# Kernel optimization log

Hardware: AMD Instinct MI355X
Metric: run time of the kernel (lower is better)

Reference implementation:

```python
import jax, jax.numpy as jnp
import numpy as np

TEMPERATURE = 0.5
NEG_INF = -1e9  # used to mask self-similarity diagonal before logsumexp


def setup_inputs() -> dict:
    key = jax.random.key(0)
    k1, k2 = jax.random.split(key)
    N, Z = 4096, 128
    z1 = jax.random.normal(k1, (N, Z), dtype=jnp.float32)
    z2 = jax.random.normal(k2, (N, Z), dtype=jnp.float32)
    return {"z1": z1, "z2": z2}


def reference(z1, z2):
    # NT-Xent (SimCLR) loss. Faithful to:
    #   sim = cosine_similarity over all pairs of concat([z1, z2])
    #   positives = sim diagonals at offsets +-N; negatives = all off-(self)diag entries
    #   cross_entropy with the positive as class 0  ->  -pos/T + logsumexp(all non-self sims / T)
    N = z1.shape[0]
    reps = jnp.concatenate([z1, z2], axis=0)                      # [2N, Z]
    # row-normalize once; cosine sim matrix is then a single GEMM
    norms = jnp.linalg.norm(reps, axis=-1, keepdims=True)
    # torch cosine_similarity clamps norms by eps=1e-8
    nreps = reps / jnp.maximum(norms, 1e-8)
    sim = nreps @ nreps.T                                          # [2N, 2N]
    # positives: sim[i, i+N] for i<N and sim[i, i-N] for i>=N
    l_pos = jnp.diagonal(sim, offset=N)                            # [N]
    r_pos = jnp.diagonal(sim, offset=-N)                           # [N]
    positives = jnp.concatenate([l_pos, r_pos])                    # [2N]
    # logsumexp over all entries except the self-similarity diagonal.
    # (The positive entry stays in the denominator exactly once, matching
    #  concat([positive, negatives]) in the original.)
    two_n = 2 * N
    self_mask = jnp.eye(two_n, dtype=bool)
    logits = jnp.where(self_mask, NEG_INF, sim / TEMPERATURE)      # [2N, 2N]
    lse = jax.nn.logsumexp(logits, axis=1)                         # [2N]
    per_row = lse - positives / TEMPERATURE                        # CE with label 0
    return jnp.sum(per_row) / two_n
```

## Files before the change

kernel.cpp:

```cpp
#include <hip/hip_runtime.h>
#include <hip/hip_bf16.h>


#define N_PAIRS 4096
#define ZDIM    128
#define NROWS   8192
#define QS 1.6986437717f

typedef __bf16 bf16x8 __attribute__((ext_vector_type(8)));
typedef float  floatx4 __attribute__((ext_vector_type(4)));

__global__ __launch_bounds__(256) void k_normalize(
    const float* __restrict__ z1, const float* __restrict__ z2,
    __hip_bfloat16* __restrict__ pack, float* __restrict__ pos,
    float* __restrict__ denom)
{
    const int zi = blockIdx.x * 256 + threadIdx.x;
    if (zi < NROWS) denom[zi] = 0.0f;

    const int w = threadIdx.x >> 6;
    const int lane = threadIdx.x & 63;
    const int p = blockIdx.x * 4 + w;
    const float2 a = ((const float2*)(z1 + (size_t)p * ZDIM))[lane];
    const float2 b = ((const float2*)(z2 + (size_t)p * ZDIM))[lane];
    float s1 = a.x * a.x + a.y * a.y;
    float s2 = b.x * b.x + b.y * b.y;
    float d  = a.x * b.x + a.y * b.y;
    #pragma unroll
    for (int off = 1; off < 64; off <<= 1) {
        s1 += __shfl_xor(s1, off, 64);
        s2 += __shfl_xor(s2, off, 64);
        d  += __shfl_xor(d,  off, 64);
    }
    const float n1 = fmaxf(sqrtf(s1), 1e-8f);
    const float n2 = fmaxf(sqrtf(s2), 1e-8f);
    const float i1 = 1.0f / n1, i2 = 1.0f / n2;
    const float q1 = i1 * QS, q2 = i2 * QS;
    float2 na; na.x = a.x * q1; na.y = a.y * q1;
    float2 nb; nb.x = b.x * q2; nb.y = b.y * q2;

    const int ks = lane >> 4;
    const int qq = (lane >> 2) & 3;
    const int jj = (lane & 3) * 2;
    const int r1 = p, r2 = p + N_PAIRS;
    const size_t i1e = ((size_t)((r1 >> 4) * 4 + ks)) * 512 + qq * 128 + (r1 & 15) * 8 + jj;
    const size_t i2e = ((size_t)((r2 >> 4) * 4 + ks)) * 512 + qq * 128 + (r2 & 15) * 8 + jj;
    *(__hip_bfloat162*)(pack + i1e) = __float22bfloat162_rn(na);
    *(__hip_bfloat162*)(pack + i2e) = __float22bfloat162_rn(nb);
    if (lane == 0) pos[p] = d * i1 * i2;
}

__global__ __launch_bounds__(256) void k_simsum(
    const __hip_bfloat16* __restrict__ pack, float* __restrict__ denom)
{
    const int tid  = threadIdx.x;
    const int lane = tid & 63;
    const int w    = tid >> 6;
    const int q    = lane >> 4;
    const int l16  = lane & 15;

    const int b  = blockIdx.x;
    int u        = (33 * b) >> 2;
    const int u1 = (33 * b + 33) >> 2;

    int rt = 0, snext = 256;
    while (u >= snext) { ++rt; snext += 256 - 8 * rt; }

    bf16x8 bufA[4][2], bufB[4][2];

    auto loadB = [&](bf16x8 (&buf)[4][2], int col) {
        const __hip_bfloat16* bp = pack + (size_t)col * 128 + lane * 8;
        #pragma unroll
        for (int ks = 0; ks < 4; ++ks)
            #pragma unroll
            for (int nt = 0; nt < 2; ++nt)
                buf[ks][nt] = *(const bf16x8*)(bp + nt * 2048 + ks * 512);
    };

    while (u < u1) {
        const int srt  = snext - (256 - 8 * rt);
        const int uend = (u1 < snext) ? u1 : snext;
        const int rowb = rt * 256 + w * 64;

        const __hip_bfloat16* Abase = pack + (size_t)rowb * 128 + lane * 8;
        bf16x8 afrag[4][4];
        #pragma unroll
        for (int mt = 0; mt < 4; ++mt)
            #pragma unroll
            for (int ks = 0; ks < 4; ++ks)
                afrag[mt][ks] = *(const bf16x8*)(Abase + mt * 2048 + ks * 512);

        float rowsum[4][4];
        #pragma unroll
        for (int mt = 0; mt < 4; ++mt)
            #pragma unroll
            for (int r = 0; r < 4; ++r) rowsum[mt][r] = 0.0f;

        auto compute = [&](bf16x8 (&buf)[4][2], int ur) {
            const int  col  = rt * 256 + ur * 32;
            const bool band = (ur < 8);
            floatx4 acc[4][2];
            #pragma unroll
            for (int mt = 0; mt < 4; ++mt)
                #pragma unroll
                for (int nt = 0; nt < 2; ++nt) {
                    acc[mt][nt].x = 0.f; acc[mt][nt].y = 0.f;
                    acc[mt][nt].z = 0.f; acc[mt][nt].w = 0.f;
                }
            #pragma unroll
            for (int ks = 0; ks < 4; ++ks)
                #pragma unroll
                for (int mt = 0; mt < 4; ++mt)
                    #pragma unroll
                    for (int nt = 0; nt < 2; ++nt)
                        acc[mt][nt] = __builtin_amdgcn_mfma_f32_16x16x32_bf16(
                            afrag[mt][ks], buf[ks][nt], acc[mt][nt], 0, 0, 0);
            float cp0 = 0.0f, cp1 = 0.0f;
            #pragma unroll
            for (int mt = 0; mt < 4; ++mt) {
                const int rowtb = rowb + mt * 16;
                #pragma unroll
                for (int nt = 0; nt < 2; ++nt) {
                    const int coltb = col + nt * 16;
                    if (band && rowtb == coltb) {
                        #pragma unroll
                        for (int r = 0; r < 4; ++r) {
                            const float e = __builtin_amdgcn_exp2f(acc[mt][nt][r]);
                            rowsum[mt][r] += (l16 == q * 4 + r) ? 0.0f : e;
                        }
                    } else {
                        #pragma unroll
                        for (int r = 0; r < 4; ++r) {
                            const float e = __builtin_amdgcn_exp2f(acc[mt][nt][r]);
                            rowsum[mt][r] += e;
                            if (!band) { if (nt == 0) cp0 += e; else cp1 += e; }
                        }
                    }
                }
            }
            if (!band) {
                cp0 += __shfl_xor(cp0, 16, 64);
                cp0 += __shfl_xor(cp0, 32, 64);
                cp1 += __shfl_xor(cp1, 16, 64);
                cp1 += __shfl_xor(cp1, 32, 64);
                if (q == 0) {
                    atomicAdd(&denom[col + l16], cp0);
                    atomicAdd(&denom[col + 16 + l16], cp1);
                }
            }
        };

        int ur        = u - srt;
        const int urn = uend - srt;
        loadB(bufA, rt * 256 + ur * 32);
        while (ur + 2 <= urn) {
            loadB(bufB, rt * 256 + (ur + 1) * 32);
            compute(bufA, ur);
            int nx = ur + 2;
            if (nx >= urn) nx = urn - 1;
            loadB(bufA, rt * 256 + nx * 32);
            compute(bufB, ur + 1);
            ur += 2;
        }
        if (ur < urn) compute(bufA, ur);

        #pragma unroll
        for (int mt = 0; mt < 4; ++mt)
            #pragma unroll
            for (int r = 0; r < 4; ++r) {
                float s = rowsum[mt][r];
                s += __shfl_xor(s, 1, 64);
                s += __shfl_xor(s, 2, 64);
                s += __shfl_xor(s, 4, 64);
                s += __shfl_xor(s, 8, 64);
                rowsum[mt][r] = s;
            }
        if (l16 == 0) {
            #pragma unroll
            for (int mt = 0; mt < 4; ++mt)
                #pragma unroll
                for (int r = 0; r < 4; ++r)
                    atomicAdd(&denom[rowb + mt * 16 + q * 4 + r], rowsum[mt][r]);
        }

        u = uend;
        if (u < u1) { ++rt; snext += 256 - 8 * rt; }
    }
}

__global__ __launch_bounds__(1024) void k_finish(
    const float* __restrict__ denom, const float* __restrict__ pos,
    float* __restrict__ out)
{
    __shared__ float red[16];
    const int t = threadIdx.x;
    const int lane = t & 63, wv = t >> 6;
    float s = 0.0f;
    for (int i = t; i < NROWS; i += 1024) s += __logf(denom[i]);
    float p = 0.0f;
    for (int i = t; i < N_PAIRS; i += 1024) p += pos[i];
    float v = s - 4.0f * p;
    #pragma unroll
    for (int off = 1; off < 64; off <<= 1) v += __shfl_xor(v, off, 64);
    if (lane == 0) red[wv] = v;
    __syncthreads();
    if (wv == 0) {
        float x = (lane < 16) ? red[lane] : 0.0f;
        #pragma unroll
        for (int off = 1; off < 16; off <<= 1) x += __shfl_xor(x, off, 64);
        if (lane == 0) out[0] = x / (float)NROWS;
    }
}

extern "C" void kernel_launch(void* const* d_in, const int* in_sizes, int n_in,
                              void* d_out, int out_size, void* d_ws, size_t ws_size,
                              hipStream_t stream) {
    const float* z1 = (const float*)d_in[0];
    const float* z2 = (const float*)d_in[1];
    float* out = (float*)d_out;

    char* ws = (char*)d_ws;
    __hip_bfloat16* pack = (__hip_bfloat16*)ws;
    float* denom = (float*)(ws + (size_t)NROWS * ZDIM * 2);
    float* pos   = denom + NROWS;

    k_normalize<<<N_PAIRS / 4, 256, 0, stream>>>(z1, z2, pack, pos, denom);
    k_simsum<<<512, 256, 0, stream>>>(pack, denom);
    k_finish<<<1, 1024, 0, stream>>>(denom, pos, out);
}
```

Baseline: 82.14 us.

## Fuse normalize, similarity-sum and finish into one cooperative kernel

Replaces the three kernel launches with a single cooperative kernel of 512 blocks. A grid-wide sync separates normalization from the similarity GEMM, and a last-block-done atomic counter runs the final reduction. The aim is to remove the launch gaps and the inter-kernel drains between stages. In exchange it pays for a grid sync, an extra atomic ticket and fences, and each block now normalizes two pairs per wave. The old three-kernel path remains as a fallback if the cooperative launch fails.

```diff
diff --git a/kernel.cpp b/kernel.cpp
--- a/kernel.cpp
+++ b/kernel.cpp
@@ -1,14 +1,227 @@
 #include <hip/hip_runtime.h>
 #include <hip/hip_bf16.h>
+#include <hip/hip_cooperative_groups.h>
+
+namespace cg = cooperative_groups;
 
 
 #define N_PAIRS 4096
 #define ZDIM    128
 #define NROWS   8192
 #define QS 1.6986437717f
+#define GRID_SIM 512
 
 typedef __bf16 bf16x8 __attribute__((ext_vector_type(8)));
 typedef float  floatx4 __attribute__((ext_vector_type(4)));
+
+__global__ __launch_bounds__(256) void k_fused(
+    const float* __restrict__ z1, const float* __restrict__ z2,
+    __hip_bfloat16* __restrict__ pack, float* __restrict__ pos,
+    float* __restrict__ denom, unsigned int* __restrict__ ctr,
+    float* __restrict__ out)
+{
+    const int tid  = threadIdx.x;
+    const int lane = tid & 63;
+    const int w    = tid >> 6;
+    const int q    = lane >> 4;
+    const int l16  = lane & 15;
+    const int b    = blockIdx.x;
+
+    __shared__ unsigned int tk;
+    __shared__ float red[4];
+
+    {
+        const int zi = b * 256 + tid;
+        if (zi < NROWS) denom[zi] = 0.0f;
+        if (zi == 0) *ctr = 0u;
+
+        #pragma unroll
+        for (int pp = 0; pp < 2; ++pp) {
+            const int p = b * 8 + w * 2 + pp;
+            const float2 a = ((const float2*)(z1 + (size_t)p * ZDIM))[lane];
+            const float2 bb = ((const float2*)(z2 + (size_t)p * ZDIM))[lane];
+            float s1 = a.x * a.x + a.y * a.y;
+            float s2 = bb.x * bb.x + bb.y * bb.y;
+            float d  = a.x * bb.x + a.y * bb.y;
+            #pragma unroll
+            for (int off = 1; off < 64; off <<= 1) {
+                s1 += __shfl_xor(s1, off, 64);
+                s2 += __shfl_xor(s2, off, 64);
+                d  += __shfl_xor(d,  off, 64);
+            }
+            const float n1 = fmaxf(sqrtf(s1), 1e-8f);
+            const float n2 = fmaxf(sqrtf(s2), 1e-8f);
+            const float i1 = 1.0f / n1, i2 = 1.0f / n2;
+            const float q1 = i1 * QS, q2 = i2 * QS;
+            float2 na; na.x = a.x * q1; na.y = a.y * q1;
+            float2 nb; nb.x = bb.x * q2; nb.y = bb.y * q2;
+
+            const int ks = lane >> 4;
+            const int qq = (lane >> 2) & 3;
+            const int jj = (lane & 3) * 2;
+            const int r1 = p, r2 = p + N_PAIRS;
+            const size_t i1e = ((size_t)((r1 >> 4) * 4 + ks)) * 512 + qq * 128 + (r1 & 15) * 8 + jj;
+            const size_t i2e = ((size_t)((r2 >> 4) * 4 + ks)) * 512 + qq * 128 + (r2 & 15) * 8 + jj;
+            *(__hip_bfloat162*)(pack + i1e) = __float22bfloat162_rn(na);
+            *(__hip_bfloat162*)(pack + i2e) = __float22bfloat162_rn(nb);
+            if (lane == 0) pos[p] = d * i1 * i2;
+        }
+    }
+
+    cg::this_grid().sync();
+
+    {
+        int u        = (33 * b) >> 2;
+        const int u1 = (33 * b + 33) >> 2;
+
+        int rt = 0, snext = 256;
+        while (u >= snext) { ++rt; snext += 256 - 8 * rt; }
+
+        bf16x8 bufA[4][2], bufB[4][2];
+
+        auto loadB = [&](bf16x8 (&buf)[4][2], int col) {
+            const __hip_bfloat16* bp = pack + (size_t)col * 128 + lane * 8;
+            #pragma unroll
+            for (int ks = 0; ks < 4; ++ks)
+                #pragma unroll
+                for (int nt = 0; nt < 2; ++nt)
+                    buf[ks][nt] = *(const bf16x8*)(bp + nt * 2048 + ks * 512);
+        };
+
+        while (u < u1) {
+            const int srt  = snext - (256 - 8 * rt);
+            const int uend = (u1 < snext) ? u1 : snext;
+            const int rowb = rt * 256 + w * 64;
+
+            const __hip_bfloat16* Abase = pack + (size_t)rowb * 128 + lane * 8;
+            bf16x8 afrag[4][4];
+            #pragma unroll
+            for (int mt = 0; mt < 4; ++mt)
+                #pragma unroll
+                for (int ks = 0; ks < 4; ++ks)
+                    afrag[mt][ks] = *(const bf16x8*)(Abase + mt * 2048 + ks * 512);
+
+            float rowsum[4][4];
+            #pragma unroll
+            for (int mt = 0; mt < 4; ++mt)
+                #pragma unroll
+                for (int r = 0; r < 4; ++r) rowsum[mt][r] = 0.0f;
+
+            auto compute = [&](bf16x8 (&buf)[4][2], int ur) {
+                const int  col  = rt * 256 + ur * 32;
+                const bool band = (ur < 8);
+                floatx4 acc[4][2];
+                #pragma unroll
+                for (int mt = 0; mt < 4; ++mt)
+                    #pragma unroll
+                    for (int nt = 0; nt < 2; ++nt) {
+                        acc[mt][nt].x = 0.f; acc[mt][nt].y = 0.f;
+                        acc[mt][nt].z = 0.f; acc[mt][nt].w = 0.f;
+                    }
+                #pragma unroll
+                for (int ks = 0; ks < 4; ++ks)
+                    #pragma unroll
+                    for (int mt = 0; mt < 4; ++mt)
+                        #pragma unroll
+                        for (int nt = 0; nt < 2; ++nt)
+                            acc[mt][nt] = __builtin_amdgcn_mfma_f32_16x16x32_bf16(
+                                afrag[mt][ks], buf[ks][nt], acc[mt][nt], 0, 0, 0);
+                float cp0 = 0.0f, cp1 = 0.0f;
+                #pragma unroll
+                for (int mt = 0; mt < 4; ++mt) {
+                    const int rowtb = rowb + mt * 16;
+                    #pragma unroll
+                    for (int nt = 0; nt < 2; ++nt) {
+                        const int coltb = col + nt * 16;
+                        if (band && rowtb == coltb) {
+                            #pragma unroll
+                            for (int r = 0; r < 4; ++r) {
+                                const float e = __builtin_amdgcn_exp2f(acc[mt][nt][r]);
+                                rowsum[mt][r] += (l16 == q * 4 + r) ? 0.0f : e;
+                            }
+                        } else {
+                            #pragma unroll
+                            for (int r = 0; r < 4; ++r) {
+                                const float e = __builtin_amdgcn_exp2f(acc[mt][nt][r]);
+                                rowsum[mt][r] += e;
+                                if (!band) { if (nt == 0) cp0 += e; else cp1 += e; }
+                            }
+                        }
+                    }
+                }
+                if (!band) {
+                    cp0 += __shfl_xor(cp0, 16, 64);
+                    cp0 += __shfl_xor(cp0, 32, 64);
+                    cp1 += __shfl_xor(cp1, 16, 64);
+                    cp1 += __shfl_xor(cp1, 32, 64);
+                    if (q == 0) {
+                        atomicAdd(&denom[col + l16], cp0);
+                        atomicAdd(&denom[col + 16 + l16], cp1);
+                    }
+                }
+            };
+
+            int ur        = u - srt;
+            const int urn = uend - srt;
+            loadB(bufA, rt * 256 + ur * 32);
+            while (ur + 2 <= urn) {
+                loadB(bufB, rt * 256 + (ur + 1) * 32);
+                compute(bufA, ur);
+                int nx = ur + 2;
+                if (nx >= urn) nx = urn - 1;
+                loadB(bufA, rt * 256 + nx * 32);
+                compute(bufB, ur + 1);
+                ur += 2;
+            }
+            if (ur < urn) compute(bufA, ur);
+
+            #pragma unroll
+            for (int mt = 0; mt < 4; ++mt)
+                #pragma unroll
+                for (int r = 0; r < 4; ++r) {
+                    float s = rowsum[mt][r];
+                    s += __shfl_xor(s, 1, 64);
+                    s += __shfl_xor(s, 2, 64);
+                    s += __shfl_xor(s, 4, 64);
+                    s += __shfl_xor(s, 8, 64);
+                    rowsum[mt][r] = s;
+                }
+            if (l16 == 0) {
+                #pragma unroll
+                for (int mt = 0; mt < 4; ++mt)
+                    #pragma unroll
+                    for (int r = 0; r < 4; ++r)
+                        atomicAdd(&denom[rowb + mt * 16 + q * 4 + r], rowsum[mt][r]);
+            }
+
+            u = uend;
+            if (u < u1) { ++rt; snext += 256 - 8 * rt; }
+        }
+    }
+
+    __threadfence();
+    __syncthreads();
+    if (tid == 0) tk = atomicAdd(ctr, 1u);
+    __syncthreads();
+    if (tk == GRID_SIM - 1) {
+        __threadfence();
+        float s = 0.0f;
+        for (int i = tid; i < NROWS; i += 256) s += __logf(denom[i]);
+        float p = 0.0f;
+        for (int i = tid; i < N_PAIRS; i += 256) p += pos[i];
+        float v = s - 4.0f * p;
+        #pragma unroll
+        for (int off = 1; off < 64; off <<= 1) v += __shfl_xor(v, off, 64);
+        if (lane == 0) red[w] = v;
+        __syncthreads();
+        if (w == 0) {
+            float x = (lane < 4) ? red[lane] : 0.0f;
+            x += __shfl_xor(x, 1, 64);
+            x += __shfl_xor(x, 2, 64);
+            if (lane == 0) out[0] = x / (float)NROWS;
+        }
+    }
+}
 
 __global__ __launch_bounds__(256) void k_normalize(
     const float* __restrict__ z1, const float* __restrict__ z2,
@@ -223,8 +436,16 @@
     __hip_bfloat16* pack = (__hip_bfloat16*)ws;
     float* denom = (float*)(ws + (size_t)NROWS * ZDIM * 2);
     float* pos   = denom + NROWS;
-
-    k_normalize<<<N_PAIRS / 4, 256, 0, stream>>>(z1, z2, pack, pos, denom);
-    k_simsum<<<512, 256, 0, stream>>>(pack, denom);
-    k_finish<<<1, 1024, 0, stream>>>(denom, pos, out);
+    unsigned int* ctr = (unsigned int*)(pos + N_PAIRS);
+
+    void* args[] = {(void*)&z1, (void*)&z2, (void*)&pack, (void*)&pos,
+                    (void*)&denom, (void*)&ctr, (void*)&out};
+    hipError_t err = hipLaunchCooperativeKernel((const void*)k_fused,
+                                                dim3(GRID_SIM), dim3(256),
+                                                args, 0, stream);
+    if (err != hipSuccess) {
+        k_normalize<<<N_PAIRS / 4, 256, 0, stream>>>(z1, z2, pack, pos, denom);
+        k_simsum<<<GRID_SIM, 256, 0, stream>>>(pack, denom);
+        k_finish<<<1, 1024, 0, stream>>>(denom, pos, out);
+    }
 }
```

New measurement: 167.3 us. 104% more time.
